# Optimization experiments

Measured on AMD Instinct MI355X. Metric: run time of the kernel, lower is better.

## Reference

```python
import jax, jax.numpy as jnp
import numpy as np

B, T, S, C, H = 2, 2048, 2048, 1024, 16
D = C // H  # head dim = 64


def setup_inputs() -> dict:
    key = jax.random.key(0)
    ks = jax.random.split(key, 6)
    sc = 1.0 / np.sqrt(C)
    return {
        "q": jax.random.normal(ks[0], (B, T, C), jnp.float32),
        "p": jax.random.normal(ks[1], (B, S, C), jnp.float32),
        "Wq": jax.random.normal(ks[2], (C, C), jnp.float32) * sc,
        "Wk": jax.random.normal(ks[3], (C, C), jnp.float32) * sc,
        "Wv": jax.random.normal(ks[4], (C, C), jnp.float32) * sc,
        "Wo": jax.random.normal(ks[5], (C, C), jnp.float32) * sc,
    }


def reference(q, p, Wq, Wk, Wv, Wo):
    # Linear projections (no bias: config.bias=True -> nn.Linear bias=False)
    qh = (q @ Wq).reshape(B, T, H, D)  # [B,T,H,D]
    kh = (p @ Wk).reshape(B, S, H, D)  # [B,S,H,D]
    vh = (p @ Wv).reshape(B, S, H, D)  # [B,S,H,D]
    scale = 1.0 / jnp.sqrt(jnp.asarray(D, qh.dtype))
    att = jnp.einsum('bthd,bshd->bhts', qh, kh) * scale  # [B,H,T,S]
    att = jax.nn.softmax(att, axis=-1)
    y = jnp.einsum('bhts,bshd->bthd', att, vh).reshape(B, T, C)
    y = y @ Wo  # c_proj, dropout p=0 (eval)
    return y
```

## Files before the change

### kernel.cpp

```cpp
#include <hip/hip_runtime.h>
#include <hip/hip_bf16.h>
#include <stdint.h>

#define T_LEN 2048
#define CDIM  1024

typedef short bf16x8_t  __attribute__((ext_vector_type(8)));
typedef float f32x4_t   __attribute__((ext_vector_type(4)));
typedef float f32x16_t  __attribute__((ext_vector_type(16)));

__device__ __forceinline__ float fexp2(float x) {
  float r;
  asm("v_exp_f32 %0, %1" : "=v"(r) : "v"(x));
  return r;
}

__device__ __forceinline__ void gload_lds16(const void* gptr, void* lptr) {
  __builtin_amdgcn_global_load_lds(
      (const __attribute__((address_space(1))) unsigned int*)(gptr),
      (__attribute__((address_space(3))) unsigned int*)(lptr),
      16, 0, 0);
}

__device__ __forceinline__ unsigned short f2bf(float f) {
  union { float f; unsigned int u; } v; v.f = f;
  unsigned int u = v.u;
  return (unsigned short)((u + 0x7fffu + ((u >> 16) & 1u)) >> 16);
}

__device__ __forceinline__ unsigned int pk_bf16(float lo, float hi) {
  unsigned int r;
  asm("v_cvt_pk_bf16_f32 %0, %1, %2" : "=v"(r) : "v"(lo), "v"(hi));
  return r;
}
__device__ __forceinline__ unsigned short bf1(float v) {
  return (unsigned short)pk_bf16(v, v);
}

__global__ __launch_bounds__(256) void cast2_f32_bf16(const float* __restrict__ x0,
                                                      const float* __restrict__ x1,
                                                      unsigned short* __restrict__ y0,
                                                      unsigned short* __restrict__ y1) {
  int i = blockIdx.x * 256 + threadIdx.x;
  const float* x = blockIdx.y ? x1 : x0;
  unsigned short* y = blockIdx.y ? y1 : y0;
  const float4* x4 = (const float4*)x;
  float4 a = x4[i * 2], b = x4[i * 2 + 1];
  union { unsigned short u[8]; uint4 v; } o;
  o.u[0] = f2bf(a.x); o.u[1] = f2bf(a.y); o.u[2] = f2bf(a.z); o.u[3] = f2bf(a.w);
  o.u[4] = f2bf(b.x); o.u[5] = f2bf(b.y); o.u[6] = f2bf(b.z); o.u[7] = f2bf(b.w);
  ((uint4*)y)[i] = o.v;
}

__global__ __launch_bounds__(256) void transpose_cast4(const float* __restrict__ W0,
                                                       const float* __restrict__ W1,
                                                       const float* __restrict__ W2,
                                                       const float* __restrict__ W3,
                                                       unsigned short* __restrict__ Wall,
                                                       unsigned short* __restrict__ Wot) {
  __shared__ float tile[32][33];
  int z = blockIdx.z;
  const float* W = (z == 0) ? W0 : (z == 1) ? W1 : (z == 2) ? W2 : W3;
  unsigned short* Wt = (z < 3) ? (Wall + (size_t)z * 1024 * 1024) : Wot;
  int tx = threadIdx.x & 31, ty = threadIdx.x >> 5;
  int n0 = blockIdx.x * 32, k0 = blockIdx.y * 32;
#pragma unroll
  for (int i = 0; i < 4; ++i) {
    int r = ty + i * 8;
    tile[r][tx] = W[(size_t)(k0 + r) * CDIM + n0 + tx];
  }
  __syncthreads();
#pragma unroll
  for (int i = 0; i < 4; ++i) {
    int r = ty + i * 8;
    Wt[(size_t)(n0 + r) * CDIM + k0 + tx] = f2bf(tile[tx][r]);
  }
}

__global__ __launch_bounds__(256) void gemm_qkv(const unsigned short* __restrict__ qbm,
                                                const unsigned short* __restrict__ pbm,
                                                const unsigned short* __restrict__ Wall,
                                                unsigned short* __restrict__ Qh,
                                                unsigned short* __restrict__ Kh,
                                                unsigned short* __restrict__ Vt) {
  __shared__ unsigned short ldsA[2][128 * 64];
  __shared__ unsigned short ldsB[2][128 * 64];
  const int tid = threadIdx.x, lane = tid & 63, w = tid >> 6;
  const int wr = w >> 1, wc = w & 1;
  const int nblk = blockIdx.x % 24, mblk = blockIdx.x / 24;
  const int m0 = mblk * 128;
  const int n0 = nblk * 128;
  const char* Ab = (const char*)((nblk < 8) ? qbm : pbm);
  const char* Bb = (const char*)Wall;
  f32x4_t acc[4][4] = {};

  auto stage = [&](int buf, int kt) {
#pragma unroll
    for (int it = 0; it < 4; ++it) {
      int ob = it * 4096 + w * 1024;
      int o = ob + lane * 16;
      int row = o >> 7, cin = o & 127;
      int cs = cin ^ ((row & 7) << 4);
      gload_lds16(Ab + (size_t)(m0 + row) * 2048 + kt * 128 + cs, (char*)ldsA[buf] + ob);
      gload_lds16(Bb + (size_t)(n0 + row) * 2048 + kt * 128 + cs, (char*)ldsB[buf] + ob);
    }
  };

  stage(0, 0);
  __syncthreads();
  int cur = 0;
  for (int kt = 0; kt < 16; ++kt) {
    if (kt < 15) stage(cur ^ 1, kt + 1);
    const char* lA = (const char*)ldsA[cur];
    const char* lB = (const char*)ldsB[cur];
#pragma unroll
    for (int kf = 0; kf < 2; ++kf) {
      int c = kf * 64 + ((lane >> 4) << 4);
      bf16x8_t af[4], bfr[4];
#pragma unroll
      for (int mf = 0; mf < 4; ++mf) {
        int row = wr * 64 + mf * 16 + (lane & 15);
        af[mf] = *(const bf16x8_t*)(lA + row * 128 + (c ^ ((row & 7) << 4)));
      }
#pragma unroll
      for (int nf = 0; nf < 4; ++nf) {
        int row = wc * 64 + nf * 16 + (lane & 15);
        bfr[nf] = *(const bf16x8_t*)(lB + row * 128 + (c ^ ((row & 7) << 4)));
      }
      __builtin_amdgcn_s_setprio(1);
#pragma unroll
      for (int mf = 0; mf < 4; ++mf)
#pragma unroll
        for (int nf = 0; nf < 4; ++nf)
          acc[mf][nf] = __builtin_amdgcn_mfma_f32_16x16x32_bf16(af[mf], bfr[nf], acc[mf][nf], 0, 0, 0);
      __builtin_amdgcn_s_setprio(0);
    }
    __syncthreads();
    cur ^= 1;
  }

  const float oscale = (nblk < 8) ? 0.18033688011112042f : 1.0f;
#pragma unroll
  for (int mf = 0; mf < 4; ++mf)
#pragma unroll
    for (int nf = 0; nf < 4; ++nf)
#pragma unroll
      for (int j = 0; j < 4; ++j) {
        int row = m0 + wr * 64 + mf * 16 + ((lane >> 4) << 2) + j;
        int col = n0 + wc * 64 + nf * 16 + (lane & 15);
        float v = acc[mf][nf][j] * oscale;
        int b = row >> 11, ts = row & 2047;
        if (col < 1024) {
          int h = col >> 6, d = col & 63;
          Qh[(((size_t)(b * 16 + h)) * 2048 + ts) * 64 + d] = bf1(v);
        } else if (col < 2048) {
          int cc = col - 1024, h = cc >> 6, d = cc & 63;
          Kh[(((size_t)(b * 16 + h)) * 2048 + ts) * 64 + d] = bf1(v);
        } else {
          int cc = col - 2048, h = cc >> 6, d = cc & 63;
          Vt[(((size_t)(b * 16 + h)) * 64 + d) * 2048 + ts] = bf1(v);
        }
      }
}

__global__ __launch_bounds__(256) void gemm_out(const unsigned short* __restrict__ A,
                                                const unsigned short* __restrict__ Bt,
                                                float* __restrict__ Out) {
  __shared__ unsigned short ldsA[2][128 * 64];
  __shared__ unsigned short ldsB[2][64 * 64];
  const int tid = threadIdx.x, lane = tid & 63, w = tid >> 6;
  const int m0 = (blockIdx.x >> 4) * 128;
  const int n0 = (blockIdx.x & 15) * 64;
  const char* Ab = (const char*)A;
  const char* Bb = (const char*)Bt;
  f32x4_t acc[2][4] = {};

  auto stage = [&](int buf, int kt) {
#pragma unroll
    for (int it = 0; it < 4; ++it) {
      int ob = it * 4096 + w * 1024;
      int o = ob + lane * 16;
      int row = o >> 7, cin = o & 127;
      int cs = cin ^ ((row & 7) << 4);
      gload_lds16(Ab + (size_t)(m0 + row) * 2048 + kt * 128 + cs, (char*)ldsA[buf] + ob);
    }
#pragma unroll
    for (int it = 0; it < 2; ++it) {
      int ob = it * 4096 + w * 1024;
      int o = ob + lane * 16;
      int row = o >> 7, cin = o & 127;
      int cs = cin ^ ((row & 7) << 4);
      gload_lds16(Bb + (size_t)(n0 + row) * 2048 + kt * 128 + cs, (char*)ldsB[buf] + ob);
    }
  };

  stage(0, 0);
  __syncthreads();
  int cur = 0;
  for (int kt = 0; kt < 16; ++kt) {
    if (kt < 15) stage(cur ^ 1, kt + 1);
    const char* lA = (const char*)ldsA[cur];
    const char* lB = (const char*)ldsB[cur];
#pragma unroll
    for (int kf = 0; kf < 2; ++kf) {
      int c = kf * 64 + ((lane >> 4) << 4);
      bf16x8_t af[2], bfr[4];
#pragma unroll
      for (int mf = 0; mf < 2; ++mf) {
        int row = w * 32 + mf * 16 + (lane & 15);
        af[mf] = *(const bf16x8_t*)(lA + row * 128 + (c ^ ((row & 7) << 4)));
      }
#pragma unroll
      for (int nf = 0; nf < 4; ++nf) {
        int row = nf * 16 + (lane & 15);
        bfr[nf] = *(const bf16x8_t*)(lB + row * 128 + (c ^ ((row & 7) << 4)));
      }
      __builtin_amdgcn_s_setprio(1);
#pragma unroll
      for (int mf = 0; mf < 2; ++mf)
#pragma unroll
        for (int nf = 0; nf < 4; ++nf)
          acc[mf][nf] = __builtin_amdgcn_mfma_f32_16x16x32_bf16(af[mf], bfr[nf], acc[mf][nf], 0, 0, 0);
      __builtin_amdgcn_s_setprio(0);
    }
    __syncthreads();
    cur ^= 1;
  }

#pragma unroll
  for (int mf = 0; mf < 2; ++mf)
#pragma unroll
    for (int nf = 0; nf < 4; ++nf)
#pragma unroll
      for (int j = 0; j < 4; ++j) {
        int row = m0 + w * 32 + mf * 16 + ((lane >> 4) << 2) + j;
        int col = n0 + nf * 16 + (lane & 15);
        Out[(size_t)row * 1024 + col] = acc[mf][nf][j];
      }
}

template <int SPLIT>
__global__ __launch_bounds__(256, 3) void attn32(const unsigned short* __restrict__ Qg,
                                                 const unsigned short* __restrict__ Kg,
                                                 const unsigned short* __restrict__ Vtg,
                                                 unsigned short* __restrict__ Ag,
                                                 float* __restrict__ OpA,
                                                 float* __restrict__ OpB,
                                                 float* __restrict__ Lp) {
  __shared__ unsigned short ldsK[3][64 * 64];
  __shared__ unsigned short ldsV[2][64 * 64];
  const int tid = threadIdx.x, lane = tid & 63, w = tid >> 6;
  const int hi = lane >> 5, ql = lane & 31;
  const int bh = blockIdx.y;
  const int q0 = blockIdx.x * 128 + w * 32;
  const int z = (SPLIT > 1) ? blockIdx.z : 0;
  constexpr int NT = 2048 / SPLIT / 64;
  const int sBeg = z * (2048 / SPLIT);

  bf16x8_t qf[4];
#pragma unroll
  for (int kd = 0; kd < 4; ++kd)
    qf[kd] = *(const bf16x8_t*)(Qg + ((size_t)bh * T_LEN + q0 + ql) * 64 + kd * 16 + hi * 8);

  bf16x8_t ones;
#pragma unroll
  for (int i = 0; i < 8; ++i) ones[i] = (short)0x3F80;

  f32x16_t oacc[2] = {};
  f32x16_t lacc = {};
  const f32x16_t vzero = {};

  const char* Kb = (const char*)(Kg + (size_t)bh * 2048 * 64);
  const char* Vb = (const char*)(Vtg + (size_t)bh * 64 * 2048);

  auto stageK = [&](int slot, int t) {
    int s0 = sBeg + t * 64;
#pragma unroll
    for (int it = 0; it < 2; ++it) {
      int ob = it * 4096 + w * 1024;
      int o = ob + lane * 16;
      int row = o >> 7, cin = o & 127;
      int cs = cin ^ ((row & 7) << 4);
      gload_lds16(Kb + (size_t)s0 * 128 + row * 128 + cs, (char*)ldsK[slot] + ob);
    }
  };
  auto stageV = [&](int slot, int t) {
    int s0 = sBeg + t * 64;
#pragma unroll
    for (int it = 0; it < 2; ++it) {
      int ob = it * 4096 + w * 1024;
      int o = ob + lane * 16;
      int row = o >> 7, cin = o & 127;
      int cs = cin ^ ((row & 7) << 4);
      gload_lds16(Vb + (size_t)s0 * 2 + (size_t)row * 4096 + cs, (char*)ldsV[slot] + ob);
    }
  };

  auto qk = [&](f32x16_t (&s)[2], int slot) {
    const char* lK = (const char*)ldsK[slot];
#pragma unroll
    for (int sub = 0; sub < 2; ++sub) {
      int row = sub * 32 + ql;
      int swz = (row & 7) << 4;
#pragma unroll
      for (int kd = 0; kd < 4; ++kd) {
        bf16x8_t kfrag = *(const bf16x8_t*)(lK + row * 128 + ((kd * 32 + hi * 16) ^ swz));
        s[sub] = __builtin_amdgcn_mfma_f32_32x32x16_bf16(kfrag, qf[kd], s[sub], 0, 0, 0);
      }
    }
  };

  auto consume = [&](f32x16_t (&s)[2], int vslot) {
    const char* lV = (const char*)ldsV[vslot];
#pragma unroll
    for (int ks = 0; ks < 4; ++ks) {
      const int sub = ks >> 1, mA = (ks & 1) * 2, mB = mA + 1;
      float e0 = fexp2(s[sub][4 * mA + 0]), e1 = fexp2(s[sub][4 * mA + 1]);
      float e2 = fexp2(s[sub][4 * mA + 2]), e3 = fexp2(s[sub][4 * mA + 3]);
      float e4 = fexp2(s[sub][4 * mB + 0]), e5 = fexp2(s[sub][4 * mB + 1]);
      float e6 = fexp2(s[sub][4 * mB + 2]), e7 = fexp2(s[sub][4 * mB + 3]);
      unsigned int a0 = pk_bf16(e0, e1), a1 = pk_bf16(e2, e3);
      unsigned int b0 = pk_bf16(e4, e5), b1 = pk_bf16(e6, e7);
      asm("v_permlane32_swap_b32 %0, %1" : "+v"(a0), "+v"(b0));
      asm("v_permlane32_swap_b32 %0, %1" : "+v"(a1), "+v"(b1));
      union { unsigned int u[4]; bf16x8_t v; } P;
      P.u[0] = a0; P.u[1] = a1; P.u[2] = b0; P.u[3] = b1;
      lacc = __builtin_amdgcn_mfma_f32_32x32x16_bf16(P.v, ones, lacc, 0, 0, 0);
#pragma unroll
      for (int dt = 0; dt < 2; ++dt) {
        int row = dt * 32 + ql;
        bf16x8_t vfrag = *(const bf16x8_t*)(lV + row * 128 + ((ks * 32 + hi * 16) ^ ((row & 7) << 4)));
        oacc[dt] = __builtin_amdgcn_mfma_f32_32x32x16_bf16(P.v, vfrag, oacc[dt], 0, 0, 0);
      }
    }
  };

  f32x16_t sA[2] = {}, sB[2] = {};
  stageK(0, 0);
  stageV(0, 0);
  stageK(1, 1);
  __syncthreads();
  qk(sA, 0);

  for (int i = 0; i < NT; i += 2) {
    if (i + 2 < NT) stageK((i + 2) % 3, i + 2);
    if (i + 1 < NT) stageV((i + 1) & 1, i + 1);
    if (i + 1 < NT) { sB[0] = vzero; sB[1] = vzero; qk(sB, (i + 1) % 3); }
    consume(sA, i & 1);
    __syncthreads();
    if (i + 1 < NT) {
      if (i + 3 < NT) stageK((i + 3) % 3, i + 3);
      if (i + 2 < NT) stageV((i + 2) & 1, i + 2);
      if (i + 2 < NT) { sA[0] = vzero; sA[1] = vzero; qk(sA, (i + 2) % 3); }
      consume(sB, (i + 1) & 1);
      __syncthreads();
    }
  }

  const int b = bh >> 4, h = bh & 15;
  if (SPLIT == 1) {
#pragma unroll
    for (int grp = 0; grp < 4; ++grp)
#pragma unroll
      for (int r2 = 0; r2 < 4; ++r2) {
        int reg = grp * 4 + r2;
        float linv = 1.0f / lacc[reg];
        int t = q0 + 4 * hi + 8 * grp + r2;
#pragma unroll
        for (int dt = 0; dt < 2; ++dt) {
          int col = h * 64 + dt * 32 + ql;
          float v = oacc[dt][reg] * linv;
          Ag[((size_t)b * T_LEN + t) * CDIM + col] = bf1(v);
        }
      }
  } else {
    float* Op = z ? OpB : OpA;
#pragma unroll
    for (int grp = 0; grp < 4; ++grp)
#pragma unroll
      for (int r2 = 0; r2 < 4; ++r2) {
        int reg = grp * 4 + r2;
        int t = q0 + 4 * hi + 8 * grp + r2;
#pragma unroll
        for (int dt = 0; dt < 2; ++dt)
          Op[((size_t)b * T_LEN + t) * CDIM + h * 64 + dt * 32 + ql] = oacc[dt][reg];
        if (ql == 0)
          Lp[(((size_t)z * 2 + b) * 16 + h) * T_LEN + t] = lacc[reg];
      }
  }
}

__global__ __launch_bounds__(256) void attn_combine(const float* __restrict__ O0,
                                                    const float* __restrict__ O1,
                                                    const float* __restrict__ Lp,
                                                    unsigned short* __restrict__ Ag) {
  int i = blockIdx.x * 256 + threadIdx.x;
  int c8 = i & 127, bt = i >> 7;
  int b = bt >> 11, t = bt & 2047;
  int c = c8 * 8, h = c >> 6;
  float l0 = Lp[(((size_t)0 * 2 + b) * 16 + h) * T_LEN + t];
  float l1 = Lp[(((size_t)1 * 2 + b) * 16 + h) * T_LEN + t];
  float inv = 1.0f / (l0 + l1);
  size_t off = (size_t)bt * CDIM + c;
  float4 x0 = *(const float4*)(O0 + off);
  float4 x1 = *(const float4*)(O1 + off);
  float4 y0 = *(const float4*)(O0 + off + 4);
  float4 y1 = *(const float4*)(O1 + off + 4);
  union { unsigned int u[4]; uint4 v; } o;
  o.u[0] = pk_bf16((x0.x + x1.x) * inv, (x0.y + x1.y) * inv);
  o.u[1] = pk_bf16((x0.z + x1.z) * inv, (x0.w + x1.w) * inv);
  o.u[2] = pk_bf16((y0.x + y1.x) * inv, (y0.y + y1.y) * inv);
  o.u[3] = pk_bf16((y0.z + y1.z) * inv, (y0.w + y1.w) * inv);
  *(uint4*)(Ag + off) = o.v;
}

extern "C" void kernel_launch(void* const* d_in, const int* in_sizes, int n_in,
                              void* d_out, int out_size, void* d_ws, size_t ws_size,
                              hipStream_t stream) {
  const float* q  = (const float*)d_in[0];
  const float* p  = (const float*)d_in[1];
  const float* Wq = (const float*)d_in[2];
  const float* Wk = (const float*)d_in[3];
  const float* Wv = (const float*)d_in[4];
  const float* Wo = (const float*)d_in[5];

  char* ws = (char*)d_ws;
  const size_t MB = (size_t)1 << 20;
  unsigned short* qb   = (unsigned short*)(ws);
  unsigned short* pb   = (unsigned short*)(ws + 8 * MB);
  unsigned short* Wall = (unsigned short*)(ws + 16 * MB);
  unsigned short* Wot  = (unsigned short*)(ws + 22 * MB);
  unsigned short* Qh   = (unsigned short*)(ws + 24 * MB);
  unsigned short* Kh   = (unsigned short*)(ws + 32 * MB);
  unsigned short* Vt   = (unsigned short*)(ws + 40 * MB);
  unsigned short* Ao   = (unsigned short*)(ws + 48 * MB);

  cast2_f32_bf16<<<dim3(2048, 2), 256, 0, stream>>>(q, p, qb, pb);
  transpose_cast4<<<dim3(32, 32, 4), 256, 0, stream>>>(Wq, Wk, Wv, Wo, Wall, Wot);

  gemm_qkv<<<768, 256, 0, stream>>>(qb, pb, Wall, Qh, Kh, Vt);

  if (ws_size >= 73 * MB) {
    float* O0 = (float*)(ws);
    float* O1 = (float*)(ws + 56 * MB);
    float* Lp = (float*)(ws + 72 * MB);
    attn32<2><<<dim3(16, 32, 2), 256, 0, stream>>>(Qh, Kh, Vt, nullptr, O0, O1, Lp);
    attn_combine<<<2048, 256, 0, stream>>>(O0, O1, Lp, Ao);
  } else {
    attn32<1><<<dim3(16, 32, 1), 256, 0, stream>>>(Qh, Kh, Vt, Ao, nullptr, nullptr, nullptr);
  }

  gemm_out<<<512, 256, 0, stream>>>(Ao, Wot, (float*)d_out);
}
```

Measured before the change: 148.1 us.

## Remap GEMM blocks per XCD and drop LDS double buffering

```diff
diff --git a/kernel.cpp b/kernel.cpp
--- a/kernel.cpp
+++ b/kernel.cpp
@@ -83,36 +83,35 @@
                                                 unsigned short* __restrict__ Qh,
                                                 unsigned short* __restrict__ Kh,
                                                 unsigned short* __restrict__ Vt) {
-  __shared__ unsigned short ldsA[2][128 * 64];
-  __shared__ unsigned short ldsB[2][128 * 64];
+  __shared__ unsigned short ldsA[128 * 64];
+  __shared__ unsigned short ldsB[128 * 64];
   const int tid = threadIdx.x, lane = tid & 63, w = tid >> 6;
   const int wr = w >> 1, wc = w & 1;
-  const int nblk = blockIdx.x % 24, mblk = blockIdx.x / 24;
+  const int bid = blockIdx.x;
+  const int xcd = bid & 7, local = bid >> 3;
+  const int pm = xcd & 3, pn = xcd >> 2;
+  const int lm = local & 7, ln = local >> 3;
+  const int mblk = pm * 8 + lm;
+  const int nblk = pn * 12 + ln;
   const int m0 = mblk * 128;
   const int n0 = nblk * 128;
   const char* Ab = (const char*)((nblk < 8) ? qbm : pbm);
   const char* Bb = (const char*)Wall;
+  char* lA = (char*)ldsA;
+  char* lB = (char*)ldsB;
   f32x4_t acc[4][4] = {};
 
-  auto stage = [&](int buf, int kt) {
+  for (int kt = 0; kt < 16; ++kt) {
 #pragma unroll
     for (int it = 0; it < 4; ++it) {
       int ob = it * 4096 + w * 1024;
       int o = ob + lane * 16;
       int row = o >> 7, cin = o & 127;
       int cs = cin ^ ((row & 7) << 4);
-      gload_lds16(Ab + (size_t)(m0 + row) * 2048 + kt * 128 + cs, (char*)ldsA[buf] + ob);
-      gload_lds16(Bb + (size_t)(n0 + row) * 2048 + kt * 128 + cs, (char*)ldsB[buf] + ob);
-    }
-  };
-
-  stage(0, 0);
-  __syncthreads();
-  int cur = 0;
-  for (int kt = 0; kt < 16; ++kt) {
-    if (kt < 15) stage(cur ^ 1, kt + 1);
-    const char* lA = (const char*)ldsA[cur];
-    const char* lB = (const char*)ldsB[cur];
+      gload_lds16(Ab + (size_t)(m0 + row) * 2048 + kt * 128 + cs, lA + ob);
+      gload_lds16(Bb + (size_t)(n0 + row) * 2048 + kt * 128 + cs, lB + ob);
+    }
+    __syncthreads();
 #pragma unroll
     for (int kf = 0; kf < 2; ++kf) {
       int c = kf * 64 + ((lane >> 4) << 4);
@@ -127,16 +126,13 @@
         int row = wc * 64 + nf * 16 + (lane & 15);
         bfr[nf] = *(const bf16x8_t*)(lB + row * 128 + (c ^ ((row & 7) << 4)));
       }
-      __builtin_amdgcn_s_setprio(1);
 #pragma unroll
       for (int mf = 0; mf < 4; ++mf)
 #pragma unroll
         for (int nf = 0; nf < 4; ++nf)
           acc[mf][nf] = __builtin_amdgcn_mfma_f32_16x16x32_bf16(af[mf], bfr[nf], acc[mf][nf], 0, 0, 0);
-      __builtin_amdgcn_s_setprio(0);
     }
     __syncthreads();
-    cur ^= 1;
   }
 
   const float oscale = (nblk < 8) ? 0.18033688011112042f : 1.0f;
@@ -166,23 +162,29 @@
 __global__ __launch_bounds__(256) void gemm_out(const unsigned short* __restrict__ A,
                                                 const unsigned short* __restrict__ Bt,
                                                 float* __restrict__ Out) {
-  __shared__ unsigned short ldsA[2][128 * 64];
-  __shared__ unsigned short ldsB[2][64 * 64];
+  __shared__ unsigned short ldsA[128 * 64];
+  __shared__ unsigned short ldsB[64 * 64];
   const int tid = threadIdx.x, lane = tid & 63, w = tid >> 6;
-  const int m0 = (blockIdx.x >> 4) * 128;
-  const int n0 = (blockIdx.x & 15) * 64;
+  const int bid = blockIdx.x;
+  const int xcd = bid & 7, local = bid >> 3;
+  const int pm = xcd & 3, pn = xcd >> 2;
+  const int lm = local & 7, ln = local >> 3;
+  const int m0 = (pm * 8 + lm) * 128;
+  const int n0 = (pn * 8 + ln) * 64;
   const char* Ab = (const char*)A;
   const char* Bb = (const char*)Bt;
+  char* lA = (char*)ldsA;
+  char* lB = (char*)ldsB;
   f32x4_t acc[2][4] = {};
 
-  auto stage = [&](int buf, int kt) {
+  for (int kt = 0; kt < 16; ++kt) {
 #pragma unroll
     for (int it = 0; it < 4; ++it) {
       int ob = it * 4096 + w * 1024;
       int o = ob + lane * 16;
       int row = o >> 7, cin = o & 127;
       int cs = cin ^ ((row & 7) << 4);
-      gload_lds16(Ab + (size_t)(m0 + row) * 2048 + kt * 128 + cs, (char*)ldsA[buf] + ob);
+      gload_lds16(Ab + (size_t)(m0 + row) * 2048 + kt * 128 + cs, lA + ob);
     }
 #pragma unroll
     for (int it = 0; it < 2; ++it) {
@@ -190,17 +192,9 @@
       int o = ob + lane * 16;
       int row = o >> 7, cin = o & 127;
       int cs = cin ^ ((row & 7) << 4);
-      gload_lds16(Bb + (size_t)(n0 + row) * 2048 + kt * 128 + cs, (char*)ldsB[buf] + ob);
-    }
-  };
-
-  stage(0, 0);
-  __syncthreads();
-  int cur = 0;
-  for (int kt = 0; kt < 16; ++kt) {
-    if (kt < 15) stage(cur ^ 1, kt + 1);
-    const char* lA = (const char*)ldsA[cur];
-    const char* lB = (const char*)ldsB[cur];
+      gload_lds16(Bb + (size_t)(n0 + row) * 2048 + kt * 128 + cs, lB + ob);
+    }
+    __syncthreads();
 #pragma unroll
     for (int kf = 0; kf < 2; ++kf) {
       int c = kf * 64 + ((lane >> 4) << 4);
@@ -215,16 +209,13 @@
         int row = nf * 16 + (lane & 15);
         bfr[nf] = *(const bf16x8_t*)(lB + row * 128 + (c ^ ((row & 7) << 4)));
       }
-      __builtin_amdgcn_s_setprio(1);
 #pragma unroll
       for (int mf = 0; mf < 2; ++mf)
 #pragma unroll
         for (int nf = 0; nf < 4; ++nf)
           acc[mf][nf] = __builtin_amdgcn_mfma_f32_16x16x32_bf16(af[mf], bfr[nf], acc[mf][nf], 0, 0, 0);
-      __builtin_amdgcn_s_setprio(0);
     }
     __syncthreads();
-    cur ^= 1;
   }
 
 #pragma unroll
```

Measured after the change: 147.0 us. About the same (-0.8%).
